# Optimization experiments

Hardware: AMD Instinct MI355X
Metric: run time of the kernel (lower is better)

## Reference

```python
import jax, jax.numpy as jnp
import numpy as np
import math

IN_DIM = 512
OUT_DIM = 512
MOD_DIM = 512
B, S = 4, 4096
EPS = 1e-8


def setup_inputs() -> dict:
    key = jax.random.key(0)
    k1, k2, k3, k4 = jax.random.split(key, 4)
    x = jax.random.normal(k1, (B, S, IN_DIM), dtype=jnp.float32)
    modulation = jax.random.normal(k2, (B, S, MOD_DIM), dtype=jnp.float32)
    # main weight: kaiming_normal_(a=0.2, fan_in, leaky_relu) -> std = sqrt(2/(1+0.2^2)) / sqrt(in_dim)
    gain = math.sqrt(2.0 / (1.0 + 0.2 ** 2))
    weight = gain / math.sqrt(IN_DIM) * jax.random.normal(k3, (OUT_DIM, IN_DIM), dtype=jnp.float32)
    bias = jnp.zeros((OUT_DIM,), dtype=jnp.float32)
    # modulation Linear: cips_bias_init -> weight ~ N(0, 1/sqrt(fan_in)), bias = 1.0
    mod_w = (1.0 / math.sqrt(MOD_DIM)) * jax.random.normal(k4, (IN_DIM, MOD_DIM), dtype=jnp.float32)
    mod_b = jnp.ones((IN_DIM,), dtype=jnp.float32)
    return {"x": x, "modulation": modulation, "weight": weight, "bias": bias,
            "mod_w": mod_w, "mod_b": mod_b}


def reference(x, modulation, weight, bias, mod_w, mod_b):
    # s = modulation linear -> per-token scale on input features  [B,S,in]
    s = jnp.einsum('bsm,im->bsi', modulation, mod_w) + mod_b
    # Algebraic rewrite of StyleGAN2 modulated linear (same math, never
    # materializes [B,S,out,in]):
    #   out[b,s,o] = sum_i (W[o,i]*s[b,s,i]*demod[b,s,o]) * x[b,s,i]
    #             = demod[b,s,o] * sum_i W[o,i] * (s*x)[b,s,i]
    #   demod = rsqrt(sum_i (W[o,i]*s[b,s,i])^2 + eps)
    out = jnp.einsum('bsi,oi->bso', x * s, weight)
    demod = jax.lax.rsqrt(jnp.einsum('bsi,oi->bso', s * s, weight * weight) + EPS)
    # torch computes demod under no_grad -> constant; irrelevant for fwd but kept explicit
    out = out * jax.lax.stop_gradient(demod) + bias
    return out
```

## Files before the change

kernel.cpp:

```cpp
#include <hip/hip_runtime.h>
#include <hip/hip_bf16.h>


#define T_TOK 16384
#define DIM 512

typedef __attribute__((ext_vector_type(4))) float f32x4;
typedef __attribute__((ext_vector_type(8))) short bf16x8;

static __device__ __forceinline__ unsigned short f2bf(float f) {
    union { float f; unsigned int u; } v; v.f = f;
    unsigned int u = v.u;
    u += 0x7fffu + ((u >> 16) & 1u);
    return (unsigned short)(u >> 16);
}
static __device__ __forceinline__ float bf2f(unsigned short h) {
    union { unsigned int u; float f; } v; v.u = ((unsigned int)h) << 16;
    return v.f;
}

__global__ __launch_bounds__(256) void k0_convert(
    const float* __restrict__ mod, const float* __restrict__ weight,
    const float* __restrict__ mod_w,
    unsigned short* __restrict__ modb, unsigned short* __restrict__ Wb,
    unsigned short* __restrict__ W2b, unsigned short* __restrict__ mwb)
{
    const int NV_MOD = (T_TOK * DIM) / 4;
    const int NV_W   = (DIM * DIM) / 4;
    int idx = blockIdx.x * blockDim.x + threadIdx.x;
    int stride = gridDim.x * blockDim.x;
    for (int i = idx; i < NV_MOD; i += stride) {
        f32x4 v = ((const f32x4*)mod)[i];
        ushort4 o; o.x = f2bf(v[0]); o.y = f2bf(v[1]); o.z = f2bf(v[2]); o.w = f2bf(v[3]);
        ((ushort4*)modb)[i] = o;
    }
    for (int i = idx; i < NV_W; i += stride) {
        f32x4 v = ((const f32x4*)weight)[i];
        ushort4 o;  o.x = f2bf(v[0]); o.y = f2bf(v[1]); o.z = f2bf(v[2]); o.w = f2bf(v[3]);
        ((ushort4*)Wb)[i] = o;
        ushort4 o2; o2.x = f2bf(v[0]*v[0]); o2.y = f2bf(v[1]*v[1]);
                    o2.z = f2bf(v[2]*v[2]); o2.w = f2bf(v[3]*v[3]);
        ((ushort4*)W2b)[i] = o2;
        f32x4 m = ((const f32x4*)mod_w)[i];
        ushort4 o3; o3.x = f2bf(m[0]); o3.y = f2bf(m[1]); o3.z = f2bf(m[2]); o3.w = f2bf(m[3]);
        ((ushort4*)mwb)[i] = o3;
    }
}

__global__ __launch_bounds__(256, 2) void k1_style(
    const unsigned short* __restrict__ modb,
    const unsigned short* __restrict__ mwb,
    const float* __restrict__ x,
    const float* __restrict__ mod_b,
    unsigned short* __restrict__ xs,
    unsigned short* __restrict__ ss)
{
    __shared__ union {
        struct { unsigned short A[128 * 64]; unsigned short B[128 * 64]; } stg;
        unsigned short str[128 * 144];
    } u;
    const int tid  = threadIdx.x;
    const int lane = tid & 63;
    const int w    = tid >> 6;
    const int wr   = w >> 1, wc = w & 1;
    const int nbn  = DIM / 128;
    const int bm   = blockIdx.x / nbn;
    const int bn   = blockIdx.x % nbn;

    const int srow  = lane >> 3;
    const int lslot = (lane & 7) ^ srow;
    const int fr    = lane & 15;
    const int fs    = lane >> 4;

    f32x4 acc[4][4] = {};

    const size_t aBase = (size_t)bm * 128 * DIM;
    const size_t bBase = (size_t)bn * 128 * DIM;

    for (int kb = 0; kb < DIM; kb += 64) {
#pragma unroll
        for (int q = 0; q < 4; ++q) {
            int row = w * 32 + q * 8 + srow;
            const unsigned short* ga = modb + aBase + (size_t)row * DIM + kb + lslot * 8;
            const unsigned short* gb = mwb  + bBase + (size_t)row * DIM + kb + lslot * 8;
            __builtin_amdgcn_global_load_lds(
                (__attribute__((address_space(1))) void*)ga,
                (__attribute__((address_space(3))) void*)(u.stg.A + w * 2048 + q * 512), 16, 0, 0);
            __builtin_amdgcn_global_load_lds(
                (__attribute__((address_space(1))) void*)gb,
                (__attribute__((address_space(3))) void*)(u.stg.B + w * 2048 + q * 512), 16, 0, 0);
        }
        __syncthreads();
#pragma unroll
        for (int kk = 0; kk < 64; kk += 32) {
            bf16x8 af[4], bfv[4];
#pragma unroll
            for (int mi = 0; mi < 4; ++mi) {
                int row = wr * 64 + mi * 16 + fr;
                int ps  = ((kk >> 3) + fs) ^ (fr & 7);
                af[mi] = *(const bf16x8*)(u.stg.A + row * 64 + ps * 8);
            }
#pragma unroll
            for (int ni = 0; ni < 4; ++ni) {
                int row = wc * 64 + ni * 16 + fr;
                int ps  = ((kk >> 3) + fs) ^ (fr & 7);
                bfv[ni] = *(const bf16x8*)(u.stg.B + row * 64 + ps * 8);
            }
#pragma unroll
            for (int mi = 0; mi < 4; ++mi)
#pragma unroll
                for (int ni = 0; ni < 4; ++ni)
                    acc[mi][ni] = __builtin_amdgcn_mfma_f32_16x16x32_bf16(
                        af[mi], bfv[ni], acc[mi][ni], 0, 0, 0);
        }
        __syncthreads();
    }

#pragma unroll
    for (int ni = 0; ni < 4; ++ni) {
        int col = wc * 64 + ni * 16 + fr;
        float mb = mod_b[bn * 128 + col];
#pragma unroll
        for (int mi = 0; mi < 4; ++mi) {
#pragma unroll
            for (int j = 0; j < 4; ++j) {
                int row = wr * 64 + mi * 16 + fs * 4 + j;
                u.str[row * 144 + col] = f2bf(acc[mi][ni][j] + mb);
            }
        }
    }
    __syncthreads();
#pragma unroll
    for (int q = 0; q < 8; ++q) {
        int row = w * 32 + q * 4 + (lane >> 4);
        int c8  = (lane & 15) * 8;
        bf16x8 s8 = *(const bf16x8*)(u.str + row * 144 + c8);
        size_t off = ((size_t)bm * 128 + row) * DIM + bn * 128 + c8;
        f32x4 x0 = *(const f32x4*)(x + off);
        f32x4 x1 = *(const f32x4*)(x + off + 4);
        bf16x8 xsv, ssv;
#pragma unroll
        for (int e = 0; e < 8; ++e) {
            float sf = bf2f((unsigned short)s8[e]);
            float xv = (e < 4) ? x0[e] : x1[e - 4];
            xsv[e] = (short)f2bf(xv * sf);
            ssv[e] = (short)f2bf(sf * sf);
        }
        *(bf16x8*)(xs + off) = xsv;
        *(bf16x8*)(ss + off) = ssv;
    }
}

__global__ __launch_bounds__(256, 3) void k2_main(
    const unsigned short* __restrict__ xs,
    const unsigned short* __restrict__ ss,
    const unsigned short* __restrict__ Wb,
    const unsigned short* __restrict__ W2b,
    const float* __restrict__ bias,
    float* __restrict__ out)
{
    __shared__ unsigned short stg[4][128 * 32];
    const int tid  = threadIdx.x;
    const int lane = tid & 63;
    const int w    = tid >> 6;
    const int wr   = w >> 1, wc = w & 1;
    const int tile = (blockIdx.x & 7) * 64 + (blockIdx.x >> 3);
    const int bm   = tile >> 2;
    const int bn   = tile & 3;

    const int fr = lane & 15;
    const int fs = lane >> 4;

    f32x4 a1[4][4] = {};
    f32x4 a2[4][4] = {};

    const size_t aBase = (size_t)bm * 128 * DIM;
    const size_t bBase = (size_t)bn * 128 * DIM;

    const int srw = lane >> 2;
    const int sp  = lane & 3;

    for (int kb = 0; kb < DIM; kb += 32) {
#pragma unroll
        for (int q = 0; q < 2; ++q) {
            int rb   = w * 32 + q * 16;
            int row  = rb + srw;
            int slog = sp ^ ((row >> 1) & 3);
            size_t gA = aBase + (size_t)row * DIM + kb + slog * 8;
            size_t gB = bBase + (size_t)row * DIM + kb + slog * 8;
            __builtin_amdgcn_global_load_lds(
                (__attribute__((address_space(1))) void*)(xs + gA),
                (__attribute__((address_space(3))) void*)(stg[0] + rb * 32), 16, 0, 0);
            __builtin_amdgcn_global_load_lds(
                (__attribute__((address_space(1))) void*)(ss + gA),
                (__attribute__((address_space(3))) void*)(stg[1] + rb * 32), 16, 0, 0);
            __builtin_amdgcn_global_load_lds(
                (__attribute__((address_space(1))) void*)(Wb + gB),
                (__attribute__((address_space(3))) void*)(stg[2] + rb * 32), 16, 0, 0);
            __builtin_amdgcn_global_load_lds(
                (__attribute__((address_space(1))) void*)(W2b + gB),
                (__attribute__((address_space(3))) void*)(stg[3] + rb * 32), 16, 0, 0);
        }
        __syncthreads();

        bf16x8 axs[4], ass[4], bw[4], bw2[4];
#pragma unroll
        for (int mi = 0; mi < 4; ++mi) {
            int row = wr * 64 + mi * 16 + fr;
            int off = row * 32 + ((fs ^ ((row >> 1) & 3)) * 8);
            axs[mi] = *(const bf16x8*)(stg[0] + off);
            ass[mi] = *(const bf16x8*)(stg[1] + off);
        }
#pragma unroll
        for (int ni = 0; ni < 4; ++ni) {
            int row = wc * 64 + ni * 16 + fr;
            int off = row * 32 + ((fs ^ ((row >> 1) & 3)) * 8);
            bw[ni]  = *(const bf16x8*)(stg[2] + off);
            bw2[ni] = *(const bf16x8*)(stg[3] + off);
        }
#pragma unroll
        for (int mi = 0; mi < 4; ++mi)
#pragma unroll
            for (int ni = 0; ni < 4; ++ni) {
                a1[mi][ni] = __builtin_amdgcn_mfma_f32_16x16x32_bf16(
                    axs[mi], bw[ni], a1[mi][ni], 0, 0, 0);
                a2[mi][ni] = __builtin_amdgcn_mfma_f32_16x16x32_bf16(
                    ass[mi], bw2[ni], a2[mi][ni], 0, 0, 0);
            }
        __syncthreads();
    }

#pragma unroll
    for (int ni = 0; ni < 4; ++ni) {
        int o = bn * 128 + wc * 64 + ni * 16 + fr;
        float bo = bias[o];
#pragma unroll
        for (int mi = 0; mi < 4; ++mi) {
#pragma unroll
            for (int j = 0; j < 4; ++j) {
                size_t t = (size_t)bm * 128 + wr * 64 + mi * 16 + fs * 4 + j;
                float d = rsqrtf(a2[mi][ni][j] + 1e-8f);
                out[t * DIM + o] = a1[mi][ni][j] * d + bo;
            }
        }
    }
}

extern "C" void kernel_launch(void* const* d_in, const int* in_sizes, int n_in,
                              void* d_out, int out_size, void* d_ws, size_t ws_size,
                              hipStream_t stream) {
    const float* x      = (const float*)d_in[0];
    const float* mod    = (const float*)d_in[1];
    const float* weight = (const float*)d_in[2];
    const float* bias   = (const float*)d_in[3];
    const float* mod_w  = (const float*)d_in[4];
    const float* mod_b  = (const float*)d_in[5];
    float* out = (float*)d_out;

    char* ws = (char*)d_ws;
    unsigned short* modb = (unsigned short*)(ws);
    unsigned short* xs   = (unsigned short*)(ws + (size_t)16777216);
    unsigned short* ssb  = (unsigned short*)(ws + (size_t)2 * 16777216);
    unsigned short* Wb   = (unsigned short*)(ws + (size_t)3 * 16777216);
    unsigned short* W2b  = (unsigned short*)(ws + (size_t)3 * 16777216 + 524288);
    unsigned short* mwb  = (unsigned short*)(ws + (size_t)3 * 16777216 + 2 * 524288);

    hipLaunchKernelGGL(k0_convert, dim3(2048), dim3(256), 0, stream,
                       mod, weight, mod_w, modb, Wb, W2b, mwb);
    hipLaunchKernelGGL(k1_style, dim3(512), dim3(256), 0, stream,
                       modb, mwb, x, mod_b, xs, ssb);
    hipLaunchKernelGGL(k2_main, dim3(512), dim3(256), 0, stream,
                       xs, ssb, Wb, W2b, bias, out);
}
```

Baseline: 60.84 us.

## Double-buffer LDS staging with async global_load_lds prefetch two tiles ahead

Splits the K loop into STAGE and COMPUTE steps over two LDS buffers. The next K-tile is loaded via global_load_lds while MFMAs run on the current one, with manual vmcnt waits and barriers. This is meant to hide global-load latency behind compute. It doubles LDS use to 64KB per block, so launch bounds drop from 3 to 2 blocks per CU, trading occupancy for overlap. The hand-counted vmcnt values could be fragile.

```diff
diff --git a/kernel.cpp b/kernel.cpp
--- a/kernel.cpp
+++ b/kernel.cpp
@@ -151,7 +151,7 @@
     }
 }
 
-__global__ __launch_bounds__(256, 3) void k2_main(
+__global__ __launch_bounds__(256, 2) void k2_main(
     const unsigned short* __restrict__ xs,
     const unsigned short* __restrict__ ss,
     const unsigned short* __restrict__ Wb,
@@ -159,7 +159,7 @@
     const float* __restrict__ bias,
     float* __restrict__ out)
 {
-    __shared__ unsigned short stg[4][128 * 32];
+    __shared__ unsigned short stg[2][4][128 * 32];
     const int tid  = threadIdx.x;
     const int lane = tid & 63;
     const int w    = tid >> 6;
@@ -180,7 +180,7 @@
     const int srw = lane >> 2;
     const int sp  = lane & 3;
 
-    for (int kb = 0; kb < DIM; kb += 32) {
+    auto STAGE = [&](int buf, int kb) {
 #pragma unroll
         for (int q = 0; q < 2; ++q) {
             int rb   = w * 32 + q * 16;
@@ -190,33 +190,34 @@
             size_t gB = bBase + (size_t)row * DIM + kb + slog * 8;
             __builtin_amdgcn_global_load_lds(
                 (__attribute__((address_space(1))) void*)(xs + gA),
-                (__attribute__((address_space(3))) void*)(stg[0] + rb * 32), 16, 0, 0);
+                (__attribute__((address_space(3))) void*)(stg[buf][0] + rb * 32), 16, 0, 0);
             __builtin_amdgcn_global_load_lds(
                 (__attribute__((address_space(1))) void*)(ss + gA),
-                (__attribute__((address_space(3))) void*)(stg[1] + rb * 32), 16, 0, 0);
+                (__attribute__((address_space(3))) void*)(stg[buf][1] + rb * 32), 16, 0, 0);
             __builtin_amdgcn_global_load_lds(
                 (__attribute__((address_space(1))) void*)(Wb + gB),
-                (__attribute__((address_space(3))) void*)(stg[2] + rb * 32), 16, 0, 0);
+                (__attribute__((address_space(3))) void*)(stg[buf][2] + rb * 32), 16, 0, 0);
             __builtin_amdgcn_global_load_lds(
                 (__attribute__((address_space(1))) void*)(W2b + gB),
-                (__attribute__((address_space(3))) void*)(stg[3] + rb * 32), 16, 0, 0);
-        }
-        __syncthreads();
-
+                (__attribute__((address_space(3))) void*)(stg[buf][3] + rb * 32), 16, 0, 0);
+        }
+    };
+
+    auto COMPUTE = [&](int buf) {
         bf16x8 axs[4], ass[4], bw[4], bw2[4];
 #pragma unroll
         for (int mi = 0; mi < 4; ++mi) {
             int row = wr * 64 + mi * 16 + fr;
             int off = row * 32 + ((fs ^ ((row >> 1) & 3)) * 8);
-            axs[mi] = *(const bf16x8*)(stg[0] + off);
-            ass[mi] = *(const bf16x8*)(stg[1] + off);
+            axs[mi] = *(const bf16x8*)(stg[buf][0] + off);
+            ass[mi] = *(const bf16x8*)(stg[buf][1] + off);
         }
 #pragma unroll
         for (int ni = 0; ni < 4; ++ni) {
             int row = wc * 64 + ni * 16 + fr;
             int off = row * 32 + ((fs ^ ((row >> 1) & 3)) * 8);
-            bw[ni]  = *(const bf16x8*)(stg[2] + off);
-            bw2[ni] = *(const bf16x8*)(stg[3] + off);
+            bw[ni]  = *(const bf16x8*)(stg[buf][2] + off);
+            bw2[ni] = *(const bf16x8*)(stg[buf][3] + off);
         }
 #pragma unroll
         for (int mi = 0; mi < 4; ++mi)
@@ -227,7 +228,27 @@
                 a2[mi][ni] = __builtin_amdgcn_mfma_f32_16x16x32_bf16(
                     ass[mi], bw2[ni], a2[mi][ni], 0, 0, 0);
             }
-        __syncthreads();
+    };
+
+    STAGE(0, 0);
+    STAGE(1, 32);
+    asm volatile("s_waitcnt vmcnt(8)" ::: "memory");
+    __builtin_amdgcn_sched_barrier(0);
+    __builtin_amdgcn_s_barrier();
+
+#pragma unroll 1
+    for (int t = 0; t < 16; ++t) {
+        int cur = t & 1;
+        COMPUTE(cur);
+        __builtin_amdgcn_s_barrier();
+        if (t <= 13) {
+            STAGE(cur, (t + 2) * 32);
+            asm volatile("s_waitcnt vmcnt(8)" ::: "memory");
+        } else if (t == 14) {
+            asm volatile("s_waitcnt vmcnt(0)" ::: "memory");
+        }
+        __builtin_amdgcn_sched_barrier(0);
+        __builtin_amdgcn_s_barrier();
     }
 
 #pragma unroll
```

Measured after the change: 58.98 us. -3.1%, faster.
